# Kernel tuning notes

Hardware: AMD Instinct MI355X
Metric: run time of the kernel (lower is better)

Reference implementation:

```python
import jax, jax.numpy as jnp
import numpy as np

# sizes
N, B, NPG = 8192, 8, 1024          # total nodes, graphs, nodes per graph (equal-size graphs)
D, H, DH, L = 256, 8, 32, 2        # hidden, heads, head dim, layers
IN_C, OUT_D, E, DFF = 128, 64, 262144, 512
EPS = 1e-5


def setup_inputs() -> dict:
    key = jax.random.key(0)
    ks = jax.random.split(key, 20)
    p = lambda i, shp: jax.random.normal(ks[i], shp, jnp.float32) * 0.05
    return dict(
        x=jax.random.normal(ks[0], (N, IN_C), jnp.float32),
        edge_index=jax.random.randint(ks[1], (2, E), 0, N),
        batch=jnp.arange(N, dtype=jnp.int32) // NPG,  # sorted, equal-size graphs
        w_in=p(2, (D, IN_C)), b_in=p(3, (D,)),
        sage_wl=p(4, (L, D, D)), sage_bl=p(5, (L, D)), sage_wr=p(6, (L, D, D)),
        attn_iw=p(7, (L, 3 * D, D)), attn_ib=p(8, (L, 3 * D)),
        attn_ow=p(9, (L, D, D)), attn_ob=p(10, (L, D)),
        n1_w=jnp.ones((L, D)), n1_b=jnp.zeros((L, D)),
        n2_w=jnp.ones((L, D)), n2_b=jnp.zeros((L, D)),
        n3_w=jnp.ones((L, D)), n3_b=jnp.zeros((L, D)),
        mlp_w1=p(11, (L, DFF, D)), mlp_b1=p(12, (L, DFF)),
        mlp_w2=p(13, (L, D, DFF)), mlp_b2=p(14, (L, D)),
        bn_w=jnp.ones((L, D)), bn_b=jnp.zeros((L, D)),
        w_out=p(15, (OUT_D, D)), b_out=p(16, (OUT_D,)),
    )


def _bn(h, w, b):
    # BatchNorm1d over nodes (training-mode batch statistics, biased var)
    m = h.mean(0)
    v = jnp.mean((h - m) ** 2, axis=0)
    return (h - m) * jax.lax.rsqrt(v + EPS) * w + b


def _forward(x, edge_index, batch, w_in, b_in, sage_wl, sage_bl, sage_wr,
             attn_iw, attn_ib, attn_ow, attn_ob, n1_w, n1_b, n2_w, n2_b,
             n3_w, n3_b, mlp_w1, mlp_b1, mlp_w2, mlp_b2, bn_w, bn_b, w_out, b_out):
    src, dst = edge_index[0], edge_index[1]
    deg = jax.ops.segment_sum(jnp.ones((E,), jnp.float32), dst, num_segments=N)
    inv_deg = (1.0 / jnp.clip(deg, 1.0))[:, None]
    scale = 1.0 / np.sqrt(DH)

    h = x @ w_in.T + b_in  # in_proj Linear  [N, D]
    for l in range(L):
        # --- GPSConv: local SAGEConv (mean aggr) + residual + norm1 ---
        agg = jax.ops.segment_sum(h[src], dst, num_segments=N) * inv_deg
        loc = agg @ sage_wl[l].T + sage_bl[l] + h @ sage_wr[l].T
        loc = _bn(loc + h, n1_w[l], n1_b[l])
        # --- GPSConv: dense per-graph multi-head self-attention + residual + norm2 ---
        hd = h.reshape(B, NPG, D)  # to_dense_batch (no padding: equal graph sizes)
        qkv = hd @ attn_iw[l].T + attn_ib[l]  # [B, n, 3D]
        q, k, v = jnp.split(qkv, 3, axis=-1)
        sh = lambda t: t.reshape(B, NPG, H, DH).transpose(0, 2, 1, 3)  # [B, H, n, DH]
        a = jax.nn.softmax(jnp.einsum('bhqd,bhkd->bhqk', sh(q) * scale, sh(k)), axis=-1)
        o = jnp.einsum('bhqk,bhkd->bhqd', a, sh(v)).transpose(0, 2, 1, 3).reshape(B, NPG, D)
        o = (o @ attn_ow[l].T + attn_ob[l]).reshape(N, D)
        glob = _bn(o + h, n2_w[l], n2_b[l])
        # --- GPSConv: sum branches, MLP residual, norm3 ---
        out = loc + glob
        out = out + jax.nn.relu(out @ mlp_w1[l].T + mlp_b1[l]) @ mlp_w2[l].T + mlp_b2[l]
        out = _bn(out, n3_w[l], n3_b[l])
        # --- outer GPS: BatchNorm + relu + (dropout=eval) + residual ---
        h = h + jax.nn.relu(_bn(out, bn_w[l], bn_b[l]))
    pooled = h.reshape(B, NPG, D).mean(axis=1)  # global_mean_pool over sorted equal-size graphs
    return pooled @ w_out.T + b_out  # [B, OUT_D]


def reference(x, edge_index, batch, w_in, b_in, sage_wl, sage_bl, sage_wr,
              attn_iw, attn_ib, attn_ow, attn_ob, n1_w, n1_b, n2_w, n2_b,
              n3_w, n3_b, mlp_w1, mlp_b1, mlp_w2, mlp_b2, bn_w, bn_b, w_out, b_out):
    return _forward(x, edge_index, batch, w_in, b_in, sage_wl, sage_bl, sage_wr,
                    attn_iw, attn_ib, attn_ow, attn_ob, n1_w, n1_b, n2_w, n2_b,
                    n3_w, n3_b, mlp_w1, mlp_b1, mlp_w2, mlp_b2, bn_w, bn_b, w_out, b_out)
```

## Files before the change

### kernel.cpp

```cpp
#include <hip/hip_runtime.h>
#include <hip/hip_bf16.h>

#define N_NODES 8192
#define BGRAPH 8
#define NPG 1024
#define DIM 256
#define NH 8
#define DHEAD 32
#define NLAYERS 2
#define INC 128
#define OUTD 64
#define NEDGE 262144
#define DFF 512
#define EPS 1e-5f

typedef __attribute__((ext_vector_type(4))) float f32x4;
typedef __attribute__((ext_vector_type(8))) short s16x8;
typedef __attribute__((ext_vector_type(4))) ushort u16x4;

__device__ __forceinline__ float b2f(ushort u){
  unsigned v = ((unsigned)u) << 16;
  return __builtin_bit_cast(float, v);
}
__device__ __forceinline__ ushort f2b(float f){
  unsigned u = __builtin_bit_cast(unsigned, f);
  u += 0x7fffu + ((u >> 16) & 1u);
  return (ushort)(u >> 16);
}
__device__ __forceinline__ ushort f2b_trunc(float f){
  return (ushort)(__builtin_bit_cast(unsigned, f) >> 16);
}
__device__ __forceinline__ void gload16(const void* g, void* l){
  __builtin_amdgcn_global_load_lds(
    (const __attribute__((address_space(1))) void*)g,
    (__attribute__((address_space(3))) void*)l,
    16, 0, 0);
}

__global__ void k_count_deg(const int* __restrict__ dst, int* __restrict__ deg){
  int i = blockIdx.x*blockDim.x + threadIdx.x;
  int stride = gridDim.x*blockDim.x;
  for(; i<NEDGE; i+=stride) atomicAdd(&deg[dst[i]], 1);
}
__global__ void k_scan(const int* __restrict__ deg, int* __restrict__ offs,
                       float* __restrict__ inv_deg){
  __shared__ int s[1024];
  int t = threadIdx.x;
  int base = t*8;
  int loc[8]; int acc=0;
  #pragma unroll
  for(int j=0;j<8;j++){
    int dv = deg[base+j];
    inv_deg[base+j] = 1.0f/(float)(dv>0?dv:1);
    loc[j]=acc; acc += dv;
  }
  s[t]=acc;
  __syncthreads();
  for(int d=1; d<1024; d<<=1){
    int v = (t>=d)? s[t-d] : 0;
    __syncthreads();
    if(t>=d) s[t]+=v;
    __syncthreads();
  }
  int pre = (t>0)? s[t-1] : 0;
  #pragma unroll
  for(int j=0;j<8;j++) offs[base+j] = pre + loc[j];
  if(t==1023) offs[N_NODES] = s[1023];
}
__global__ void k_fill_csr(const int* __restrict__ src, const int* __restrict__ dst,
                           const int* __restrict__ offs, int* __restrict__ cursor,
                           int* __restrict__ csr){
  int i = blockIdx.x*blockDim.x + threadIdx.x;
  int stride = gridDim.x*blockDim.x;
  for(; i<NEDGE; i+=stride){
    int d = dst[i];
    int p = atomicAdd(&cursor[d], 1);
    csr[offs[d]+p] = src[i];
  }
}

__global__ __launch_bounds__(256) void k_aggregate(ushort* __restrict__ hwb,
    const int* __restrict__ offs, const int* __restrict__ csr,
    const float* __restrict__ inv_deg){
  int n = blockIdx.x*4 + (threadIdx.x>>6);
  int lane = threadIdx.x & 63;
  int beg = offs[n], end = offs[n+1];
  f32x4 a0 = {0,0,0,0}, a1 = {0,0,0,0}, a2 = {0,0,0,0}, a3 = {0,0,0,0};
  int i = beg;
  for(; i+4<=end; i+=4){
    int j0=csr[i], j1=csr[i+1], j2=csr[i+2], j3=csr[i+3];
    u16x4 v0 = *(const u16x4*)(hwb + (size_t)j0*512 + 256 + lane*4);
    u16x4 v1 = *(const u16x4*)(hwb + (size_t)j1*512 + 256 + lane*4);
    u16x4 v2 = *(const u16x4*)(hwb + (size_t)j2*512 + 256 + lane*4);
    u16x4 v3 = *(const u16x4*)(hwb + (size_t)j3*512 + 256 + lane*4);
    #pragma unroll
    for(int c=0;c<4;c++){ a0[c]+=b2f(v0[c]); a1[c]+=b2f(v1[c]);
                          a2[c]+=b2f(v2[c]); a3[c]+=b2f(v3[c]); }
  }
  for(; i<end; ++i){
    int j0=csr[i];
    u16x4 v0 = *(const u16x4*)(hwb + (size_t)j0*512 + 256 + lane*4);
    #pragma unroll
    for(int c=0;c<4;c++) a0[c]+=b2f(v0[c]);
  }
  float inv = inv_deg[n];
  u16x4 outv;
  #pragma unroll
  for(int c=0;c<4;c++) outv[c] = f2b((a0[c]+a1[c]+a2[c]+a3[c])*inv);
  *(u16x4*)(hwb + (size_t)n*512 + lane*4) = outv;
}

#define STAGE_AB(t, buf) do{ \
    int kt_ = (t)*64; \
    _Pragma("unroll") \
    for(int it=0; it<2; ++it){ \
      int c = (wave*2+it)*64 + lane; \
      int row = c >> 3, q = c & 7; \
      int qs = q ^ (row & 7); \
      gload16(A + (size_t)(bm+row)*lda + kt_ + qs*8, (char*)As + (buf)*8192 + (wave*2+it)*1024); \
      gload16(W + (size_t)(bn+row)*K   + kt_ + qs*8, (char*)Bs + (buf)*8192 + (wave*2+it)*1024); \
    } \
  }while(0)

template<bool RELU, bool RESID, bool RESIDB, bool BIAS, bool WF32, bool WBF, bool STATS>
__global__ __launch_bounds__(256) void k_mm(const ushort* __restrict__ A,
    const ushort* __restrict__ W, const float* __restrict__ bias,
    const float* __restrict__ resid, const ushort* __restrict__ residb,
    float* __restrict__ Cf, ushort* __restrict__ Cb,
    float* __restrict__ gS, float* __restrict__ gQ,
    int M, int Nc, int K, int lda, int ldcb)
{
  __shared__ ushort As[2*64*64];
  __shared__ ushort Bs[2*64*64];
  __shared__ float sredS[64];
  __shared__ float sredQ[64];
  const int tid = threadIdx.x;
  const int lane = tid & 63, wave = tid >> 6;
  const int l15 = lane & 15, l4 = lane >> 4;
  const int bm = blockIdx.y*64, bn = blockIdx.x*64;
  const int wr = wave >> 1, wc = wave & 1;
  f32x4 acc[2][2] = {};
  const int nt = K >> 6;

  STAGE_AB(0, 0);
  asm volatile("s_waitcnt vmcnt(0)" ::: "memory");
  __builtin_amdgcn_s_barrier();

  int cur = 0;
  for(int t=0; t<nt; ++t){
    if(t+1 < nt) STAGE_AB(t+1, cur^1);
    #pragma unroll
    for(int kk=0; kk<2; ++kk){
      s16x8 af[2], bfr[2];
      #pragma unroll
      for(int mi=0; mi<2; ++mi){
        int row = wr*32 + mi*16 + l15;
        int col = (kk*64 + l4*16) ^ ((row & 7) << 4);
        af[mi] = *(const s16x8*)((const char*)As + cur*8192 + row*128 + col);
      }
      #pragma unroll
      for(int nj=0; nj<2; ++nj){
        int row = wc*32 + nj*16 + l15;
        int col = (kk*64 + l4*16) ^ ((row & 7) << 4);
        bfr[nj] = *(const s16x8*)((const char*)Bs + cur*8192 + row*128 + col);
      }
      #pragma unroll
      for(int mi=0; mi<2; ++mi)
        #pragma unroll
        for(int nj=0; nj<2; ++nj)
          acc[mi][nj] = __builtin_amdgcn_mfma_f32_16x16x32_bf16(af[mi], bfr[nj], acc[mi][nj], 0,0,0);
    }
    asm volatile("s_waitcnt vmcnt(0)" ::: "memory");
    __builtin_amdgcn_s_barrier();
    cur ^= 1;
  }

  float sloc[2] = {0.f,0.f}, qloc[2] = {0.f,0.f};
  #pragma unroll
  for(int mi=0; mi<2; ++mi){
    #pragma unroll
    for(int nj=0; nj<2; ++nj){
      int col = bn + wc*32 + nj*16 + l15;
      float bv = BIAS ? bias[col] : 0.f;
      #pragma unroll
      for(int r=0; r<4; ++r){
        int row = bm + wr*32 + mi*16 + l4*4 + r;
        size_t off = (size_t)row*Nc + col;
        float v = acc[mi][nj][r] + bv;
        if(RESID)  v += resid[off];
        if(RESIDB) v += b2f(residb[off]);
        if(RELU)   v = fmaxf(v, 0.f);
        if(WF32)   Cf[off] = v;
        if(WBF)    Cb[(size_t)row*ldcb + col] = f2b(v);
        if(STATS){ sloc[nj] += v; qloc[nj] += v*v; }
      }
    }
  }
  if(STATS){
    if(tid < 64){ sredS[tid]=0.f; sredQ[tid]=0.f; }
    __syncthreads();
    int c0 = wc*32 + l15;
    atomicAdd(&sredS[c0],    sloc[0]); atomicAdd(&sredQ[c0],    qloc[0]);
    atomicAdd(&sredS[c0+16], sloc[1]); atomicAdd(&sredQ[c0+16], qloc[1]);
    __syncthreads();
    if(tid < 64){
      atomicAdd(&gS[bn+tid], sredS[tid]);
      atomicAdd(&gQ[bn+tid], sredQ[tid]);
    }
  }
}

__global__ __launch_bounds__(256) void k_attn(const ushort* __restrict__ qkv,
                                              ushort* __restrict__ attnO)
{
  __shared__ ushort Ks[64*32];
  __shared__ ushort Vt[32*64];
  const int tid = threadIdx.x, lane = tid & 63, wave = tid >> 6;
  const int l15 = lane & 15, g = lane >> 4;
  int bid = blockIdx.x;
  int qc = bid & 15;
  int h  = (bid >> 4) & 7;
  int bg = bid >> 7;
  const int nb = bg*NPG + qc*64 + wave*16;
  const int kb = bg*NPG;

  s16x8 qf = *(const s16x8*)(qkv + (size_t)(nb + l15)*768 + h*32 + g*8);
  {
    const float scale2 = 0.2550370703637335f;
    #pragma unroll
    for(int i=0;i<8;i++) qf[i] = (short)f2b(b2f((ushort)qf[i]) * scale2);
  }
  f32x4 o0 = {0.f,0.f,0.f,0.f}, o1 = {0.f,0.f,0.f,0.f};
  float mrun = -1e30f, lrun = 0.f;

  for(int st=0; st<16; ++st){
    __syncthreads();
    {
      int rho = tid >> 2, q = tid & 3;
      int grp = rho >> 5, r32 = rho & 31;
      int tt = r32 >> 4, wi = r32 & 15;
      int j = grp*32 + (wi >> 2)*8 + tt*4 + (wi & 3);
      int qs = q ^ ((rho >> 1) & 3);
      const ushort* gp = qkv + (size_t)(kb + st*64 + j)*768 + 256 + h*32 + qs*8;
      gload16(gp, (char*)Ks + wave*1024);
    }
    {
      int j = lane;
      s16x8 vv = *(const s16x8*)(qkv + (size_t)(kb + st*64 + j)*768 + 512 + h*32 + wave*8);
      #pragma unroll
      for(int i=0;i<8;i++){
        int d = wave*8 + i;
        Vt[d*64 + (j ^ (i<<3))] = (ushort)vv[i];
      }
    }
    __syncthreads();

    f32x4 sc[4];
    __builtin_amdgcn_s_setprio(1);
    #pragma unroll
    for(int q4=0; q4<4; ++q4){
      int rho = q4*16 + l15;
      s16x8 kf = *(const s16x8*)((const char*)Ks + rho*64 + ((g*16) ^ (((rho>>1)&3)<<4)));
      f32x4 z = {0.f,0.f,0.f,0.f};
      sc[q4] = __builtin_amdgcn_mfma_f32_16x16x32_bf16(kf, qf, z, 0,0,0);
    }
    __builtin_amdgcn_s_setprio(0);

    float smax = -1e30f;
    #pragma unroll
    for(int q4=0; q4<4; ++q4)
      #pragma unroll
      for(int r=0; r<4; ++r) smax = fmaxf(smax, sc[q4][r]);
    smax = fmaxf(smax, __shfl_xor(smax, 16));
    smax = fmaxf(smax, __shfl_xor(smax, 32));

    if(!__all((int)(smax <= mrun + 8.0f))){
      float mnew = fmaxf(mrun, smax);
      float alpha = exp2f(mrun - mnew);
      lrun *= alpha;
      #pragma unroll
      for(int r=0;r<4;r++){
        float ar = __shfl(alpha, (lane & 48) | (g*4 + r), 64);
        o0[r] *= ar; o1[r] *= ar;
      }
      mrun = mnew;
    }

    float p[16];
    float ps = 0.f;
    #pragma unroll
    for(int q4=0; q4<4; ++q4)
      #pragma unroll
      for(int r=0; r<4; ++r){
        float pv = exp2f(sc[q4][r] - mrun);
        p[q4*4+r] = pv; ps += pv;
      }
    ps += __shfl_xor(ps, 16);
    ps += __shfl_xor(ps, 32);
    lrun += ps;

    s16x8 pa0, pa1;
    #pragma unroll
    for(int i=0;i<8;i++){ pa0[i] = (short)f2b_trunc(p[i]); pa1[i] = (short)f2b_trunc(p[8+i]); }

    int colb0 = g*16, colb1 = 64 + g*16;
    int d0 = l15, d1 = l15 + 16;
    s16x8 v00 = *(const s16x8*)((const char*)Vt + d0*128 + (colb0 ^ ((d0&7)<<4)));
    s16x8 v01 = *(const s16x8*)((const char*)Vt + d1*128 + (colb0 ^ ((d1&7)<<4)));
    s16x8 v10 = *(const s16x8*)((const char*)Vt + d0*128 + (colb1 ^ ((d0&7)<<4)));
    s16x8 v11 = *(const s16x8*)((const char*)Vt + d1*128 + (colb1 ^ ((d1&7)<<4)));
    __builtin_amdgcn_s_setprio(1);
    o0 = __builtin_amdgcn_mfma_f32_16x16x32_bf16(pa0, v00, o0, 0,0,0);
    o1 = __builtin_amdgcn_mfma_f32_16x16x32_bf16(pa0, v01, o1, 0,0,0);
    o0 = __builtin_amdgcn_mfma_f32_16x16x32_bf16(pa1, v10, o0, 0,0,0);
    o1 = __builtin_amdgcn_mfma_f32_16x16x32_bf16(pa1, v11, o1, 0,0,0);
    __builtin_amdgcn_s_setprio(0);
  }
  float inv = 1.0f/lrun;
  #pragma unroll
  for(int r=0;r<4;r++){
    int q2 = g*4 + r;
    float ir = __shfl(inv, (lane & 48) | q2, 64);
    size_t nrow = (size_t)(nb + q2)*DIM + h*32;
    attnO[nrow + l15]      = f2b(o0[r]*ir);
    attnO[nrow + 16 + l15] = f2b(o1[r]*ir);
  }
}

__global__ __launch_bounds__(256) void k_apply12(const float* __restrict__ locC,
    const float* __restrict__ globC, const float* __restrict__ slot,
    const float* __restrict__ n1w, const float* __restrict__ n1b,
    const float* __restrict__ n2w, const float* __restrict__ n2b,
    ushort* __restrict__ combB){
  int d = threadIdx.x;
  size_t i = (size_t)blockIdx.x*DIM + d;
  const float invn = 1.0f/N_NODES;
  float m1 = slot[d]*invn,     v1 = slot[256+d]*invn - m1*m1;
  float m2 = slot[512+d]*invn, v2 = slot[768+d]*invn - m2*m2;
  float rs1 = rsqrtf(v1+EPS), rs2 = rsqrtf(v2+EPS);
  float y1 = (locC[i]-m1)*rs1*n1w[d] + n1b[d];
  float y2 = (globC[i]-m2)*rs2*n2w[d] + n2b[d];
  combB[i] = f2b(y1 + y2);
}

__global__ __launch_bounds__(256) void k_apply3o(const float* __restrict__ x,
    const float* __restrict__ slot, const float* __restrict__ n3w,
    const float* __restrict__ n3b, const float* __restrict__ bw,
    const float* __restrict__ bb, float* __restrict__ H,
    ushort* __restrict__ hwbR){
  int d = threadIdx.x;
  size_t i = (size_t)blockIdx.x*DIM + d;
  const float invn = 1.0f/N_NODES;
  float m   = slot[1024+d]*invn;
  float var = slot[1280+d]*invn - m*m;
  float rs  = rsqrtf(var+EPS);
  float gch = rs*n3w[d];
  float rso = rsqrtf(gch*gch*var + EPS);
  float yo = (x[i]-m)*gch*rso*bw[d] + bb[d];
  float h = H[i] + fmaxf(yo, 0.f);
  H[i] = h;
  hwbR[(size_t)blockIdx.x*512 + d] = f2b(h);
}

#define CX  1048576
#define CWI (CX+32768)
#define CSW (CWI+262144)
#define CIW (CSW+393216)
#define COW (CIW+131072)
#define CW1 (COW+262144)
#define CW2 (CW1+262144)
__global__ void k_cast_all(const float* __restrict__ x, const float* __restrict__ w_in,
    const float* __restrict__ wl, const float* __restrict__ wr,
    const float* __restrict__ iw, const float* __restrict__ ow,
    const float* __restrict__ w1, const float* __restrict__ w2,
    ushort* __restrict__ dst){
  int i = blockIdx.x*256 + threadIdx.x;
  float val;
  if(i < CX)       val = x[i];
  else if(i < CWI) val = w_in[i-CX];
  else if(i < CSW){
    int j = i - CWI;
    int l = j >> 17, r = (j >> 9) & 255, k = j & 511;
    val = (k < 256) ? wl[(l<<16) + (r<<8) + k] : wr[(l<<16) + (r<<8) + (k-256)];
  }
  else if(i < CIW) val = iw[i-CSW];
  else if(i < COW) val = ow[i-CIW];
  else if(i < CW1) val = w1[i-COW];
  else             val = w2[i-CW1];
  dst[i] = f2b(val);
}

__global__ void k_pool(const float* __restrict__ h, float* __restrict__ pooled){
  int b = blockIdx.x, c = blockIdx.y, d = threadIdx.x;
  int r0 = c*64;
  float s=0.f;
  for(int i=0;i<64;i++) s += h[(size_t)(b*NPG + r0 + i)*DIM + d];
  atomicAdd(&pooled[b*DIM+d], s*(1.0f/NPG));
}
__global__ void k_out(const float* __restrict__ pooled, const float* __restrict__ w_out,
                      const float* __restrict__ b_out, float* __restrict__ out){
  int t = threadIdx.x;
  if(t >= BGRAPH*OUTD) return;
  int b = t/OUTD, oc = t%OUTD;
  float s = b_out[oc];
  for(int k=0;k<DIM;k++) s += pooled[b*DIM+k]*w_out[oc*DIM+k];
  out[t] = s;
}

extern "C" void kernel_launch(void* const* d_in, const int* in_sizes, int n_in,
                              void* d_out, int out_size, void* d_ws, size_t ws_size,
                              hipStream_t stream) {
  const float* x       = (const float*)d_in[0];
  const int*   edge    = (const int*)d_in[1];
  const float* w_in    = (const float*)d_in[3];
  const float* b_in    = (const float*)d_in[4];
  const float* sage_wl = (const float*)d_in[5];
  const float* sage_bl = (const float*)d_in[6];
  const float* sage_wr = (const float*)d_in[7];
  const float* attn_iw = (const float*)d_in[8];
  const float* attn_ib = (const float*)d_in[9];
  const float* attn_ow = (const float*)d_in[10];
  const float* attn_ob = (const float*)d_in[11];
  const float* n1_w = (const float*)d_in[12];
  const float* n1_b = (const float*)d_in[13];
  const float* n2_w = (const float*)d_in[14];
  const float* n2_b = (const float*)d_in[15];
  const float* n3_w = (const float*)d_in[16];
  const float* n3_b = (const float*)d_in[17];
  const float* mlp_w1 = (const float*)d_in[18];
  const float* mlp_b1 = (const float*)d_in[19];
  const float* mlp_w2 = (const float*)d_in[20];
  const float* mlp_b2 = (const float*)d_in[21];
  const float* bn_w = (const float*)d_in[22];
  const float* bn_b = (const float*)d_in[23];
  const float* w_out = (const float*)d_in[24];
  const float* b_out = (const float*)d_in[25];

  const size_t ND = (size_t)N_NODES*DIM;
  float* ws    = (float*)d_ws;
  float* H     = ws;
  float* locC  = ws + ND;
  float* globC = ws + 2*ND;
  ushort* wsb   = (ushort*)(ws + 3*ND);
  ushort* hwb   = wsb;
  ushort* qkvb  = wsb + 2*ND;
  ushort* attnOb= wsb + 5*ND;
  ushort* combb = wsb + 6*ND;
  ushort* hidb  = wsb + 7*ND;
  ushort* castb = wsb + 9*ND;
  ushort* xb     = castb;
  ushort* w_in_b = castb + CX;
  ushort* sageWb = castb + CWI;
  ushort* iw_b   = castb + CSW;
  ushort* ow_b   = castb + CIW;
  ushort* w1_b   = castb + COW;
  ushort* w2_b   = castb + CW1;
  float* mf      = (float*)(castb + CW2);
  float* inv_deg = mf;
  float* bnslots = mf + 8192;
  float* pooled  = bnslots + 3072;
  int* deg    = (int*)(pooled + 2048);
  int* cursor = deg + N_NODES;
  int* offs   = cursor + N_NODES;
  int* csr    = offs + N_NODES + 8;

  const int* esrc = edge;
  const int* edst = edge + NEDGE;

  hipMemsetAsync(bnslots, 0, (3072+2048)*sizeof(float) + 2*N_NODES*sizeof(int), stream);

  k_count_deg<<<512,256,0,stream>>>(edst, deg);
  k_scan<<<1,1024,0,stream>>>(deg, offs, inv_deg);
  k_fill_csr<<<512,256,0,stream>>>(esrc, edst, offs, cursor, csr);
  k_cast_all<<<CW2/256,256,0,stream>>>(x, w_in, sage_wl, sage_wr, attn_iw,
      attn_ow, mlp_w1, mlp_w2, castb);

  k_mm<false,false,false,true,true,true,false><<<dim3(4,128),256,0,stream>>>(
      xb, w_in_b, b_in, nullptr, nullptr, H, hwb+256, nullptr, nullptr,
      N_NODES, DIM, INC, INC, 512);

  for(int l=0; l<NLAYERS; ++l){
    const ushort* swb = sageWb + (size_t)l*131072;
    const ushort* iwb = iw_b + (size_t)l*196608;
    const ushort* owb = ow_b + (size_t)l*65536;
    const ushort* w1b = w1_b + (size_t)l*131072;
    const ushort* w2b = w2_b + (size_t)l*131072;
    float* slot = bnslots + (size_t)l*1536;

    k_aggregate<<<N_NODES/4,256,0,stream>>>(hwb, offs, csr, inv_deg);
    k_mm<false,true,false,true,true,false,true><<<dim3(4,128),256,0,stream>>>(
        hwb, swb, sage_bl + l*DIM, H, nullptr, locC, nullptr, slot, slot+256,
        N_NODES, DIM, 512, 512, 0);

    k_mm<false,false,false,true,false,true,false><<<dim3(12,128),256,0,stream>>>(
        hwb+256, iwb, attn_ib + l*3*DIM, nullptr, nullptr, nullptr, qkvb,
        nullptr, nullptr, N_NODES, 3*DIM, DIM, 512, 768);
    k_attn<<<1024,256,0,stream>>>(qkvb, attnOb);
    k_mm<false,true,false,true,true,false,true><<<dim3(4,128),256,0,stream>>>(
        attnOb, owb, attn_ob + l*DIM, H, nullptr, globC, nullptr, slot+512, slot+768,
        N_NODES, DIM, DIM, DIM, 0);

    k_apply12<<<N_NODES,256,0,stream>>>(locC, globC, slot,
        n1_w + l*DIM, n1_b + l*DIM, n2_w + l*DIM, n2_b + l*DIM, combb);

    k_mm<true,false,false,true,false,true,false><<<dim3(8,128),256,0,stream>>>(
        combb, w1b, mlp_b1 + l*DFF, nullptr, nullptr, nullptr, hidb,
        nullptr, nullptr, N_NODES, DFF, DIM, DIM, 512);
    k_mm<false,false,true,true,true,false,true><<<dim3(4,128),256,0,stream>>>(
        hidb, w2b, mlp_b2 + l*DIM, nullptr, combb, globC, nullptr,
        slot+1024, slot+1280, N_NODES, DIM, 512, 512, 0);

    k_apply3o<<<N_NODES,256,0,stream>>>(globC, slot, n3_w + l*DIM, n3_b + l*DIM,
        bn_w + l*DIM, bn_b + l*DIM, H, hwb+256);
  }

  k_pool<<<dim3(BGRAPH, NPG/64),256,0,stream>>>(H, pooled);
  k_out<<<1,512,0,stream>>>(pooled, w_out, b_out, (float*)d_out);
}
```

Baseline: 310.1 us.

## Triple-buffer GEMM tiles and double-buffer K/V staging in attention

The GEMM kernel moves from two to three LDS stages and uses partial vmcnt waits, so two tiles' global loads are in flight while the current tile is computed. The attention kernel double-buffers its K and transposed-V shared tiles and prefetches the next block's K and V into registers and LDS during compute, with one barrier before use and one after. Both aim to hide global-load latency behind MFMA work. The cost is more LDS per block, which may lower occupancy, and the hand-counted vmcnt values are fragile if the compiler reorders or splits loads.

```diff
diff --git a/kernel.cpp b/kernel.cpp
--- a/kernel.cpp
+++ b/kernel.cpp
@@ -130,8 +130,8 @@
     float* __restrict__ gS, float* __restrict__ gQ,
     int M, int Nc, int K, int lda, int ldcb)
 {
-  __shared__ ushort As[2*64*64];
-  __shared__ ushort Bs[2*64*64];
+  __shared__ ushort As[3*64*64];
+  __shared__ ushort Bs[3*64*64];
   __shared__ float sredS[64];
   __shared__ float sredQ[64];
   const int tid = threadIdx.x;
@@ -143,12 +143,19 @@
   const int nt = K >> 6;
 
   STAGE_AB(0, 0);
-  asm volatile("s_waitcnt vmcnt(0)" ::: "memory");
-  __builtin_amdgcn_s_barrier();
-
-  int cur = 0;
+  if(nt > 1) STAGE_AB(1, 1);
+
   for(int t=0; t<nt; ++t){
-    if(t+1 < nt) STAGE_AB(t+1, cur^1);
+    int cb = t % 3;
+    if(t+2 < nt){
+      STAGE_AB(t+2, (t+2)%3);
+      asm volatile("s_waitcnt vmcnt(8)" ::: "memory");
+    } else if(t+1 < nt){
+      asm volatile("s_waitcnt vmcnt(4)" ::: "memory");
+    } else {
+      asm volatile("s_waitcnt vmcnt(0)" ::: "memory");
+    }
+    __builtin_amdgcn_s_barrier();
     #pragma unroll
     for(int kk=0; kk<2; ++kk){
       s16x8 af[2], bfr[2];
@@ -156,13 +163,13 @@
       for(int mi=0; mi<2; ++mi){
         int row = wr*32 + mi*16 + l15;
         int col = (kk*64 + l4*16) ^ ((row & 7) << 4);
-        af[mi] = *(const s16x8*)((const char*)As + cur*8192 + row*128 + col);
+        af[mi] = *(const s16x8*)((const char*)As + cb*8192 + row*128 + col);
       }
       #pragma unroll
       for(int nj=0; nj<2; ++nj){
         int row = wc*32 + nj*16 + l15;
         int col = (kk*64 + l4*16) ^ ((row & 7) << 4);
-        bfr[nj] = *(const s16x8*)((const char*)Bs + cur*8192 + row*128 + col);
+        bfr[nj] = *(const s16x8*)((const char*)Bs + cb*8192 + row*128 + col);
       }
       #pragma unroll
       for(int mi=0; mi<2; ++mi)
@@ -170,9 +177,8 @@
         for(int nj=0; nj<2; ++nj)
           acc[mi][nj] = __builtin_amdgcn_mfma_f32_16x16x32_bf16(af[mi], bfr[nj], acc[mi][nj], 0,0,0);
     }
-    asm volatile("s_waitcnt vmcnt(0)" ::: "memory");
+    asm volatile("s_waitcnt lgkmcnt(0)" ::: "memory");
     __builtin_amdgcn_s_barrier();
-    cur ^= 1;
   }
 
   float sloc[2] = {0.f,0.f}, qloc[2] = {0.f,0.f};
@@ -213,8 +219,8 @@
 __global__ __launch_bounds__(256) void k_attn(const ushort* __restrict__ qkv,
                                               ushort* __restrict__ attnO)
 {
-  __shared__ ushort Ks[64*32];
-  __shared__ ushort Vt[32*64];
+  __shared__ ushort Ks[2][64*32];
+  __shared__ ushort Vt[2][32*64];
   const int tid = threadIdx.x, lane = tid & 63, wave = tid >> 6;
   const int l15 = lane & 15, g = lane >> 4;
   int bid = blockIdx.x;
@@ -224,6 +230,12 @@
   const int nb = bg*NPG + qc*64 + wave*16;
   const int kb = bg*NPG;
 
+  const int rho = tid >> 2, qq = tid & 3;
+  const int grp = rho >> 5, r32 = rho & 31;
+  const int tt = r32 >> 4, wi = r32 & 15;
+  const int jperm = grp*32 + (wi >> 2)*8 + tt*4 + (wi & 3);
+  const int qs = qq ^ ((rho >> 1) & 3);
+
   s16x8 qf = *(const s16x8*)(qkv + (size_t)(nb + l15)*768 + h*32 + g*8);
   {
     const float scale2 = 0.2550370703637335f;
@@ -233,34 +245,33 @@
   f32x4 o0 = {0.f,0.f,0.f,0.f}, o1 = {0.f,0.f,0.f,0.f};
   float mrun = -1e30f, lrun = 0.f;
 
+  gload16(qkv + (size_t)(kb + jperm)*768 + 256 + h*32 + qs*8, (char*)Ks[0] + wave*1024);
+  s16x8 vcur = *(const s16x8*)(qkv + (size_t)(kb + lane)*768 + 512 + h*32 + wave*8);
+
   for(int st=0; st<16; ++st){
-    __syncthreads();
-    {
-      int rho = tid >> 2, q = tid & 3;
-      int grp = rho >> 5, r32 = rho & 31;
-      int tt = r32 >> 4, wi = r32 & 15;
-      int j = grp*32 + (wi >> 2)*8 + tt*4 + (wi & 3);
-      int qs = q ^ ((rho >> 1) & 3);
-      const ushort* gp = qkv + (size_t)(kb + st*64 + j)*768 + 256 + h*32 + qs*8;
-      gload16(gp, (char*)Ks + wave*1024);
-    }
-    {
-      int j = lane;
-      s16x8 vv = *(const s16x8*)(qkv + (size_t)(kb + st*64 + j)*768 + 512 + h*32 + wave*8);
-      #pragma unroll
-      for(int i=0;i<8;i++){
-        int d = wave*8 + i;
-        Vt[d*64 + (j ^ (i<<3))] = (ushort)vv[i];
-      }
-    }
-    __syncthreads();
+    int buf = st & 1;
+    #pragma unroll
+    for(int i=0;i<8;i++){
+      int d = wave*8 + i;
+      Vt[buf][d*64 + (lane ^ (i<<3))] = (ushort)vcur[i];
+    }
+    s16x8 vnext = vcur;
+    if(st+1 < 16){
+      gload16(qkv + (size_t)(kb + (st+1)*64 + jperm)*768 + 256 + h*32 + qs*8,
+              (char*)Ks[buf^1] + wave*1024);
+      vnext = *(const s16x8*)(qkv + (size_t)(kb + (st+1)*64 + lane)*768 + 512 + h*32 + wave*8);
+      asm volatile("s_waitcnt vmcnt(2) lgkmcnt(0)" ::: "memory");
+    } else {
+      asm volatile("s_waitcnt vmcnt(0) lgkmcnt(0)" ::: "memory");
+    }
+    __builtin_amdgcn_s_barrier();
 
     f32x4 sc[4];
     __builtin_amdgcn_s_setprio(1);
     #pragma unroll
     for(int q4=0; q4<4; ++q4){
-      int rho = q4*16 + l15;
-      s16x8 kf = *(const s16x8*)((const char*)Ks + rho*64 + ((g*16) ^ (((rho>>1)&3)<<4)));
+      int r0 = q4*16 + l15;
+      s16x8 kf = *(const s16x8*)((const char*)Ks[buf] + r0*64 + ((g*16) ^ (((r0>>1)&3)<<4)));
       f32x4 z = {0.f,0.f,0.f,0.f};
       sc[q4] = __builtin_amdgcn_mfma_f32_16x16x32_bf16(kf, qf, z, 0,0,0);
     }
@@ -305,16 +316,20 @@
 
     int colb0 = g*16, colb1 = 64 + g*16;
     int d0 = l15, d1 = l15 + 16;
-    s16x8 v00 = *(const s16x8*)((const char*)Vt + d0*128 + (colb0 ^ ((d0&7)<<4)));
-    s16x8 v01 = *(const s16x8*)((const char*)Vt + d1*128 + (colb0 ^ ((d1&7)<<4)));
-    s16x8 v10 = *(const s16x8*)((const char*)Vt + d0*128 + (colb1 ^ ((d0&7)<<4)));
-    s16x8 v11 = *(const s16x8*)((const char*)Vt + d1*128 + (colb1 ^ ((d1&7)<<4)));
+    s16x8 v00 = *(const s16x8*)((const char*)Vt[buf] + d0*128 + (colb0 ^ ((d0&7)<<4)));
+    s16x8 v01 = *(const s16x8*)((const char*)Vt[buf] + d1*128 + (colb0 ^ ((d1&7)<<4)));
+    s16x8 v10 = *(const s16x8*)((const char*)Vt[buf] + d0*128 + (colb1 ^ ((d0&7)<<4)));
+    s16x8 v11 = *(const s16x8*)((const char*)Vt[buf] + d1*128 + (colb1 ^ ((d1&7)<<4)));
     __builtin_amdgcn_s_setprio(1);
     o0 = __builtin_amdgcn_mfma_f32_16x16x32_bf16(pa0, v00, o0, 0,0,0);
     o1 = __builtin_amdgcn_mfma_f32_16x16x32_bf16(pa0, v01, o1, 0,0,0);
     o0 = __builtin_amdgcn_mfma_f32_16x16x32_bf16(pa1, v10, o0, 0,0,0);
     o1 = __builtin_amdgcn_mfma_f32_16x16x32_bf16(pa1, v11, o1, 0,0,0);
     __builtin_amdgcn_s_setprio(0);
+
+    asm volatile("s_waitcnt lgkmcnt(0)" ::: "memory");
+    __builtin_amdgcn_s_barrier();
+    vcur = vnext;
   }
   float inv = 1.0f/lrun;
   #pragma unroll
```

Measured after the change: 314.2 us. No clear change (+1.3%).
